# Optimization experiments

Hardware: AMD Instinct MI355X
Metric: run time of the kernel (lower is better)

## Reference

```python
import jax, jax.numpy as jnp
import numpy as np

C_IN = 128
C_INNER = 128


def setup_inputs() -> dict:
    key = jax.random.key(0)
    ks = jax.random.split(key, 9)
    b, c, h, w = 4, C_IN, 64, 64
    s = 1.0 / np.sqrt(c)
    x = jax.random.normal(ks[0], (b, c, h, w), dtype=jnp.float32)
    Wq = jax.random.normal(ks[1], (C_INNER, C_IN), dtype=jnp.float32) * s
    bq = jnp.zeros((C_INNER,), dtype=jnp.float32)
    Wk = jax.random.normal(ks[2], (C_INNER, C_IN), dtype=jnp.float32) * s
    bk = jnp.zeros((C_INNER,), dtype=jnp.float32)
    Wv = jax.random.normal(ks[3], (C_INNER, C_IN), dtype=jnp.float32) * s
    bv = jnp.zeros((C_INNER,), dtype=jnp.float32)
    Wo = jax.random.normal(ks[4], (C_IN, C_INNER), dtype=jnp.float32) * (1.0 / np.sqrt(C_INNER))
    bo = jnp.zeros((C_IN,), dtype=jnp.float32)
    return {"x": x, "Wq": Wq, "bq": bq, "Wk": Wk, "bk": bk,
            "Wv": Wv, "bv": bv, "Wo": Wo, "bo": bo}


def _conv1x1(x, W, bias):
    # x: (b,c,h,w), W: (o,c) -> (b,o,h,w)
    return jnp.einsum('oc,bchw->bohw', W, x) + bias[None, :, None, None]


def reference(x, Wq, bq, Wk, bk, Wv, bv, Wo, bo):
    b, c, h, w = x.shape
    ci = Wq.shape[0]
    n = h * w
    q = _conv1x1(x, Wq, bq).reshape(b, ci, n)          # (b, ci, n)
    k = _conv1x1(x, Wk, bk).reshape(b, ci, n)          # (b, ci, n)
    v = _conv1x1(x, Wv, bv).reshape(b, ci, n)          # (b, ci, n)
    # attn = softmax(q^T @ k) over keys
    attn = jnp.einsum('bci,bcj->bij', q, k)            # (b, n, n)
    attn = jax.nn.softmax(attn, axis=-1)
    out = jnp.einsum('bij,bcj->bci', attn, v)          # (b, ci, n)
    out = out.reshape(b, ci, h, w)
    out = _conv1x1(out, Wo, bo)
    return out + x
```

## Files before the change

### kernel.cpp

```cpp
#include <hip/hip_runtime.h>
#include <math.h>
#include <stdint.h>

#define CDIM 128
#define NTOT 4096

typedef _Float16 f16x8 __attribute__((ext_vector_type(8)));
typedef float floatx4 __attribute__((ext_vector_type(4)));

static __device__ __forceinline__ floatx4 mfma16(f16x8 a, f16x8 b, floatx4 c) {
    return __builtin_amdgcn_mfma_f32_16x16x32_f16(a, b, c, 0, 0, 0);
}
static __device__ __forceinline__ unsigned short f2h(float f) {
    _Float16 h = (_Float16)f;
    return __builtin_bit_cast(unsigned short, h);
}
static __device__ __forceinline__ float h2f(unsigned short u) {
    return (float)__builtin_bit_cast(_Float16, u);
}

#define SWZ(row, cc) ((((row) << 7)) + ((((cc) ^ ((row) & 15))) << 3))

__global__ __launch_bounds__(256) void qkv_proj_kernel(
    const float* __restrict__ x,
    const float* __restrict__ Wq, const float* __restrict__ bq,
    const float* __restrict__ Wk, const float* __restrict__ bk,
    const float* __restrict__ Wv, const float* __restrict__ bv,
    unsigned short* __restrict__ qo, unsigned short* __restrict__ ko,
    unsigned short* __restrict__ vo)
{
    __shared__ __align__(16) unsigned short Xs[64][136];
    __shared__ __align__(16) unsigned short Ws[64][136];

    const int t = threadIdx.x, b = blockIdx.y, n0 = blockIdx.x * 64;
    const int zo = blockIdx.z * 64;
    const int w = t >> 6, quad = (t >> 4) & 3, l15 = t & 15;

    {
        const int n = (t & 15) * 4;
        const int c = (t >> 4) * 8;
        float4 xr[8];
        #pragma unroll
        for (int j = 0; j < 8; ++j)
            xr[j] = *(const float4*)&x[((size_t)b * CDIM + c + j) * NTOT + n0 + n];
        #pragma unroll
        for (int k = 0; k < 4; ++k) {
            ushort4 ulo, uhi;
            ulo.x = f2h(((const float*)&xr[0])[k]);
            ulo.y = f2h(((const float*)&xr[1])[k]);
            ulo.z = f2h(((const float*)&xr[2])[k]);
            ulo.w = f2h(((const float*)&xr[3])[k]);
            uhi.x = f2h(((const float*)&xr[4])[k]);
            uhi.y = f2h(((const float*)&xr[5])[k]);
            uhi.z = f2h(((const float*)&xr[6])[k]);
            uhi.w = f2h(((const float*)&xr[7])[k]);
            *(ushort4*)&Xs[n + k][c]     = ulo;
            *(ushort4*)&Xs[n + k][c + 4] = uhi;
        }
    }

    f16x8 xf[4];
    for (int s = 0; s < 3; ++s) {
        const float* W    = (s == 0) ? Wq : (s == 1) ? Wk : Wv;
        const float* bias = (s == 0) ? bq : (s == 1) ? bk : bv;
        if (s) __syncthreads();
        {
            int o = t >> 2, ch = (t & 3) * 32;
            #pragma unroll
            for (int i = 0; i < 8; ++i) {
                float4 f4 = *(const float4*)&W[(size_t)(zo + o) * CDIM + ch + i * 4];
                ushort4 u = { f2h(f4.x), f2h(f4.y), f2h(f4.z), f2h(f4.w) };
                *(ushort4*)&Ws[o][ch + i * 4] = u;
            }
        }
        __syncthreads();
        if (s == 0) {
            #pragma unroll
            for (int f = 0; f < 4; ++f)
                xf[f] = *(const f16x8*)&Xs[w * 16 + l15][f * 32 + quad * 8];
        }

        if (s < 2) {
            unsigned short* dst = (s == 0) ? qo : ko;
            #pragma unroll
            for (int ot = 0; ot < 4; ++ot) {
                floatx4 acc = (floatx4){0.f, 0.f, 0.f, 0.f};
                #pragma unroll
                for (int f = 0; f < 4; ++f) {
                    f16x8 aW = *(const f16x8*)&Ws[ot * 16 + l15][f * 32 + quad * 8];
                    acc = mfma16(aW, xf[f], acc);
                }
                const int ob = zo + ot * 16 + quad * 4;
                ushort4 u;
                u.x = f2h(acc[0] + bias[ob + 0]);
                u.y = f2h(acc[1] + bias[ob + 1]);
                u.z = f2h(acc[2] + bias[ob + 2]);
                u.w = f2h(acc[3] + bias[ob + 3]);
                *(ushort4*)&dst[((size_t)b * NTOT + n0 + w * 16 + l15) * CDIM + ob] = u;
            }
        } else {
            #pragma unroll
            for (int ot = 0; ot < 4; ++ot) {
                floatx4 acc = (floatx4){0.f, 0.f, 0.f, 0.f};
                #pragma unroll
                for (int f = 0; f < 4; ++f) {
                    f16x8 bW = *(const f16x8*)&Ws[ot * 16 + l15][f * 32 + quad * 8];
                    acc = mfma16(xf[f], bW, acc);
                }
                const int o = zo + ot * 16 + l15;
                const float bv_ = bias[o];
                ushort4 u;
                u.x = f2h(acc[0] + bv_); u.y = f2h(acc[1] + bv_);
                u.z = f2h(acc[2] + bv_); u.w = f2h(acc[3] + bv_);
                *(ushort4*)&vo[((size_t)b * CDIM + o) * NTOT + n0 + w * 16 + quad * 4] = u;
            }
        }
    }
}

__global__ __launch_bounds__(256, 2) void attn_kernel(
    const unsigned short* __restrict__ qg,
    const unsigned short* __restrict__ kg,
    const unsigned short* __restrict__ vg,
    unsigned short* __restrict__ Op,
    float* __restrict__ Ms, float* __restrict__ Ls)
{
    __shared__ __align__(16) unsigned short Ks[128 * 128];
    __shared__ __align__(16) unsigned short Vs[128 * 128];

    const int t = threadIdx.x;
    const int w = t >> 6, quad = (t >> 4) & 3, l15 = t & 15;
    const int b = blockIdx.y;
    const int z = blockIdx.z;
    const int i0 = blockIdx.x * 128;
    const int jbase = z * 1024;
    const size_t vbase = (size_t)b * CDIM * NTOT;

    f16x8 bQ[2][4];
    #pragma unroll
    for (int nt = 0; nt < 2; ++nt) {
        const size_t qrow = ((size_t)b * NTOT + i0 + w * 32 + nt * 16 + l15) * CDIM;
        #pragma unroll
        for (int f = 0; f < 4; ++f)
            bQ[nt][f] = *(const f16x8*)&qg[qrow + f * 32 + quad * 8];
    }

    floatx4 accO[2][8];
    #pragma unroll
    for (int nt = 0; nt < 2; ++nt)
        #pragma unroll
        for (int dt = 0; dt < 8; ++dt) accO[nt][dt] = (floatx4){0.f, 0.f, 0.f, 0.f};
    float m_run[2] = {-INFINITY, -INFINITY};
    float l_part[2] = {0.f, 0.f};

    for (int iter = 0; iter < 8; ++iter) {
        const int j0 = jbase + iter * 128;
        __syncthreads();

        {
            const size_t kb_ = ((size_t)b * NTOT + j0) * CDIM;
            #pragma unroll
            for (int r = 0; r < 8; ++r) {
                int flat = r * 256 + t;
                int row = flat >> 4, cc = flat & 15;
                *(uint4*)&Ks[SWZ(row, cc)] =
                    *(const uint4*)&kg[kb_ + (size_t)row * CDIM + cc * 8];
                *(uint4*)&Vs[SWZ(row, cc)] =
                    *(const uint4*)&vg[vbase + (size_t)row * NTOT + j0 + cc * 8];
            }
        }
        __syncthreads();

        floatx4 accT[2][8];
        #pragma unroll
        for (int nt = 0; nt < 2; ++nt)
            #pragma unroll
            for (int jt = 0; jt < 8; ++jt) accT[nt][jt] = (floatx4){0.f, 0.f, 0.f, 0.f};
        #pragma unroll
        for (int jt = 0; jt < 8; ++jt)
            #pragma unroll
            for (int f = 0; f < 4; ++f) {
                f16x8 aK = *(const f16x8*)&Ks[SWZ(jt * 16 + l15, f * 4 + quad)];
                accT[0][jt] = mfma16(aK, bQ[0][f], accT[0][jt]);
                accT[1][jt] = mfma16(aK, bQ[1][f], accT[1][jt]);
            }

        float m_new[2], alpha[2];
        ushort4 pu[2][8];
        #pragma unroll
        for (int nt = 0; nt < 2; ++nt) {
            float tm = accT[nt][0][0];
            #pragma unroll
            for (int jt = 0; jt < 8; ++jt)
                #pragma unroll
                for (int r = 0; r < 4; ++r) tm = fmaxf(tm, accT[nt][jt][r]);
            tm = fmaxf(tm, __shfl_xor(tm, 16));
            tm = fmaxf(tm, __shfl_xor(tm, 32));
            m_new[nt] = fmaxf(m_run[nt], tm);
            alpha[nt] = __expf(m_run[nt] - m_new[nt]);
            m_run[nt] = m_new[nt];
            float ps = 0.f;
            #pragma unroll
            for (int jt = 0; jt < 8; ++jt) {
                float p0 = __expf(accT[nt][jt][0] - m_new[nt]);
                float p1 = __expf(accT[nt][jt][1] - m_new[nt]);
                float p2 = __expf(accT[nt][jt][2] - m_new[nt]);
                float p3 = __expf(accT[nt][jt][3] - m_new[nt]);
                ps += (p0 + p1) + (p2 + p3);
                pu[nt][jt].x = f2h(p0); pu[nt][jt].y = f2h(p1);
                pu[nt][jt].z = f2h(p2); pu[nt][jt].w = f2h(p3);
            }
            l_part[nt] = l_part[nt] * alpha[nt] + ps;
            #pragma unroll
            for (int dt = 0; dt < 8; ++dt) {
                accO[nt][dt][0] *= alpha[nt]; accO[nt][dt][1] *= alpha[nt];
                accO[nt][dt][2] *= alpha[nt]; accO[nt][dt][3] *= alpha[nt];
            }
        }

        __syncthreads();

        #pragma unroll
        for (int nt = 0; nt < 2; ++nt) {
            const int prow = w * 32 + nt * 16 + l15;
            #pragma unroll
            for (int jt = 0; jt < 8; ++jt)
                *(ushort4*)&Ks[SWZ(prow, 2 * jt + (quad >> 1)) + (quad & 1) * 4] =
                    pu[nt][jt];
        }

        f16x8 bP[2][4];
        #pragma unroll
        for (int nt = 0; nt < 2; ++nt) {
            const int prow = w * 32 + nt * 16 + l15;
            #pragma unroll
            for (int kb = 0; kb < 4; ++kb)
                bP[nt][kb] = *(const f16x8*)&Ks[SWZ(prow, kb * 4 + quad)];
        }
        #pragma unroll
        for (int dt = 0; dt < 8; ++dt)
            #pragma unroll
            for (int kb = 0; kb < 4; ++kb) {
                f16x8 aV = *(const f16x8*)&Vs[SWZ(dt * 16 + l15, kb * 4 + quad)];
                accO[0][dt] = mfma16(aV, bP[0][kb], accO[0][dt]);
                accO[1][dt] = mfma16(aV, bP[1][kb], accO[1][dt]);
            }
    }

    #pragma unroll
    for (int nt = 0; nt < 2; ++nt) {
        float lf = l_part[nt];
        lf += __shfl_xor(lf, 16);
        lf += __shfl_xor(lf, 32);
        const float inv = 1.0f / lf;
        const size_t orow =
            (((size_t)z * 4 + b) * NTOT + i0 + w * 32 + nt * 16 + l15) * CDIM;
        #pragma unroll
        for (int dt = 0; dt < 8; ++dt) {
            ushort4 u;
            u.x = f2h(accO[nt][dt][0] * inv); u.y = f2h(accO[nt][dt][1] * inv);
            u.z = f2h(accO[nt][dt][2] * inv); u.w = f2h(accO[nt][dt][3] * inv);
            *(ushort4*)&Op[orow + dt * 16 + quad * 4] = u;
        }
        if (quad == 0) {
            const int idx = (z * 4 + b) * NTOT + i0 + w * 32 + nt * 16 + l15;
            Ms[idx] = m_run[nt];
            Ls[idx] = lf;
        }
    }
}

__global__ __launch_bounds__(256) void out_proj_kernel(
    const unsigned short* __restrict__ Op,
    const float* __restrict__ Ms, const float* __restrict__ Ls,
    const float* __restrict__ Wo, const float* __restrict__ bo,
    const float* __restrict__ x, float* __restrict__ out)
{
    __shared__ __align__(16) unsigned short As[64][136];
    __shared__ __align__(16) unsigned short Ws[64][136];

    const int t = threadIdx.x, b = blockIdx.y, n0 = blockIdx.x * 64;
    const int zo = blockIdx.z * 64;
    const int w = t >> 6, quad = (t >> 4) & 3, l15 = t & 15;

    const size_t PER = (size_t)NTOT * 4 * CDIM;

    #pragma unroll
    for (int r = 0; r < 4; ++r) {
        int flat = r * 256 + t;
        int row = flat >> 4, c16 = (flat & 15) * 8;
        const int bn = b * NTOT + n0 + row;
        float m0 = Ms[bn], m1 = Ms[bn + 16384], m2 = Ms[bn + 32768], m3 = Ms[bn + 49152];
        float M = fmaxf(fmaxf(m0, m1), fmaxf(m2, m3));
        float w0 = Ls[bn]         * __expf(m0 - M);
        float w1 = Ls[bn + 16384] * __expf(m1 - M);
        float w2 = Ls[bn + 32768] * __expf(m2 - M);
        float w3 = Ls[bn + 49152] * __expf(m3 - M);
        const float inv = 1.0f / (w0 + w1 + w2 + w3);
        w0 *= inv; w1 *= inv; w2 *= inv; w3 *= inv;

        const size_t base = (size_t)bn * CDIM + c16;
        uint4 a0 = *(const uint4*)&Op[base];
        uint4 a1 = *(const uint4*)&Op[PER + base];
        uint4 a2 = *(const uint4*)&Op[2 * PER + base];
        uint4 a3 = *(const uint4*)&Op[3 * PER + base];
        const unsigned short* p0 = (const unsigned short*)&a0;
        const unsigned short* p1 = (const unsigned short*)&a1;
        const unsigned short* p2 = (const unsigned short*)&a2;
        const unsigned short* p3 = (const unsigned short*)&a3;
        unsigned short mv[8];
        #pragma unroll
        for (int j = 0; j < 8; ++j)
            mv[j] = f2h(w0 * h2f(p0[j]) + w1 * h2f(p1[j]) +
                        w2 * h2f(p2[j]) + w3 * h2f(p3[j]));
        *(uint4*)&As[row][c16] = *(const uint4*)mv;
    }
    {
        int o = t >> 2, ch = (t & 3) * 32;
        #pragma unroll
        for (int i = 0; i < 8; ++i) {
            float4 f4 = *(const float4*)&Wo[(size_t)(zo + o) * CDIM + ch + i * 4];
            ushort4 u = { f2h(f4.x), f2h(f4.y), f2h(f4.z), f2h(f4.w) };
            *(ushort4*)&Ws[o][ch + i * 4] = u;
        }
    }
    __syncthreads();

    f16x8 bA[4];
    #pragma unroll
    for (int f = 0; f < 4; ++f)
        bA[f] = *(const f16x8*)&As[w * 16 + l15][f * 32 + quad * 8];

    #pragma unroll
    for (int ot = 0; ot < 4; ++ot) {
        floatx4 acc = (floatx4){0.f, 0.f, 0.f, 0.f};
        #pragma unroll
        for (int f = 0; f < 4; ++f) {
            f16x8 aW = *(const f16x8*)&Ws[ot * 16 + l15][f * 32 + quad * 8];
            acc = mfma16(aW, bA[f], acc);
        }
        const int ob = zo + ot * 16 + quad * 4;
        #pragma unroll
        for (int r = 0; r < 4; ++r) {
            size_t idx = ((size_t)b * CDIM + ob + r) * NTOT + n0 + w * 16 + l15;
            out[idx] = acc[r] + bo[ob + r] + x[idx];
        }
    }
}

extern "C" void kernel_launch(void* const* d_in, const int* in_sizes, int n_in,
                              void* d_out, int out_size, void* d_ws, size_t ws_size,
                              hipStream_t stream)
{
    const float* x  = (const float*)d_in[0];
    const float* Wq = (const float*)d_in[1];
    const float* bq = (const float*)d_in[2];
    const float* Wk = (const float*)d_in[3];
    const float* bk = (const float*)d_in[4];
    const float* Wv = (const float*)d_in[5];
    const float* bv = (const float*)d_in[6];
    const float* Wo = (const float*)d_in[7];
    const float* bo = (const float*)d_in[8];
    float* out = (float*)d_out;

    const size_t PER = (size_t)4 * CDIM * NTOT;
    unsigned short* q_ws  = (unsigned short*)d_ws;
    unsigned short* k_ws  = q_ws + PER;
    unsigned short* v_ws  = k_ws + PER;
    unsigned short* op_ws = v_ws + PER;
    float*          ms_ws = (float*)(op_ws + 4 * PER);
    float*          ls_ws = ms_ws + 4 * 16384;

    qkv_proj_kernel<<<dim3(64, 4, 2), dim3(256), 0, stream>>>(
        x, Wq, bq, Wk, bk, Wv, bv, q_ws, k_ws, v_ws);
    attn_kernel<<<dim3(32, 4, 4), dim3(256), 0, stream>>>(
        q_ws, k_ws, v_ws, op_ws, ms_ws, ls_ws);
    out_proj_kernel<<<dim3(64, 4, 2), dim3(256), 0, stream>>>(
        op_ws, ms_ws, ls_ws, Wo, bo, x, out);
}
```

Measured before the change: 165.3 us.

## Double-buffer K/V tiles with async global-to-LDS loads and remap attention grid

The attention kernel now stages 64-key K/V tiles into two LDS buffers using global_load_lds direct copies, prefetching the next tile while computing on the current one, instead of synchronous 128-key loads through registers. The tile size halves so the loop runs 16 iterations, with a new 8-wide swizzle for the 64-column V and P layouts. The grid is flattened to 1D with a block-index swizzle to improve L2 locality across batches and key splits. The aim is to hide global-load latency and cut register staging, at the cost of more barriers and smaller MFMA work per iteration.

New measurement: 144.3 us. 12.7% less time.

```diff
diff --git a/kernel.cpp b/kernel.cpp
--- a/kernel.cpp
+++ b/kernel.cpp
@@ -20,6 +20,13 @@
 }
 
 #define SWZ(row, cc) ((((row) << 7)) + ((((cc) ^ ((row) & 15))) << 3))
+#define SWZ8(row, cc) ((((row) << 6)) + ((((cc) ^ ((row) & 7))) << 3))
+
+static __device__ __forceinline__ void gload_lds16(const void* g, void* l) {
+    __builtin_amdgcn_global_load_lds(
+        (const __attribute__((address_space(1))) void*)g,
+        (__attribute__((address_space(3))) void*)l, 16, 0, 0);
+}
 
 __global__ __launch_bounds__(256) void qkv_proj_kernel(
     const float* __restrict__ x,
@@ -125,14 +132,18 @@
     unsigned short* __restrict__ Op,
     float* __restrict__ Ms, float* __restrict__ Ls)
 {
-    __shared__ __align__(16) unsigned short Ks[128 * 128];
-    __shared__ __align__(16) unsigned short Vs[128 * 128];
+    __shared__ __align__(16) unsigned short Kb[2][64 * 128];
+    __shared__ __align__(16) unsigned short Vb[2][128 * 64];
 
     const int t = threadIdx.x;
     const int w = t >> 6, quad = (t >> 4) & 3, l15 = t & 15;
-    const int b = blockIdx.y;
-    const int z = blockIdx.z;
-    const int i0 = blockIdx.x * 128;
+
+    const int bid = blockIdx.x;
+    const int swz = ((bid & 7) << 6) | (bid >> 3);
+    const int gidx = swz >> 5;
+    const int b = gidx & 3;
+    const int z = gidx >> 2;
+    const int i0 = (swz & 31) * 128;
     const int jbase = z * 1024;
     const size_t vbase = (size_t)b * CDIM * NTOT;
 
@@ -144,6 +155,22 @@
         for (int f = 0; f < 4; ++f)
             bQ[nt][f] = *(const f16x8*)&qg[qrow + f * 32 + quad * 8];
     }
+
+    auto stage = [&](unsigned short* Kd, unsigned short* Vd, int j0) {
+        const size_t kbase = ((size_t)b * NTOT + j0) * CDIM;
+        const size_t vrow0 = vbase + j0;
+        #pragma unroll
+        for (int r = 0; r < 4; ++r) {
+            const int flat = r * 256 + t;
+            const int ldsoff = (r * 256 + (t & ~63)) * 8;
+            const int krow = flat >> 4, kcc = flat & 15;
+            gload_lds16(&kg[kbase + (size_t)krow * CDIM + ((kcc ^ (krow & 15)) << 3)],
+                        &Kd[ldsoff]);
+            const int vrow = flat >> 3, vcc = flat & 7;
+            gload_lds16(&vg[vrow0 + (size_t)vrow * NTOT + ((vcc ^ (vrow & 7)) << 3)],
+                        &Vd[ldsoff]);
+        }
+    };
 
     floatx4 accO[2][8];
     #pragma unroll
@@ -153,45 +180,37 @@
     float m_run[2] = {-INFINITY, -INFINITY};
     float l_part[2] = {0.f, 0.f};
 
-    for (int iter = 0; iter < 8; ++iter) {
-        const int j0 = jbase + iter * 128;
-        __syncthreads();
-
-        {
-            const size_t kb_ = ((size_t)b * NTOT + j0) * CDIM;
-            #pragma unroll
-            for (int r = 0; r < 8; ++r) {
-                int flat = r * 256 + t;
-                int row = flat >> 4, cc = flat & 15;
-                *(uint4*)&Ks[SWZ(row, cc)] =
-                    *(const uint4*)&kg[kb_ + (size_t)row * CDIM + cc * 8];
-                *(uint4*)&Vs[SWZ(row, cc)] =
-                    *(const uint4*)&vg[vbase + (size_t)row * NTOT + j0 + cc * 8];
-            }
-        }
-        __syncthreads();
-
-        floatx4 accT[2][8];
+    stage(Kb[0], Vb[0], jbase);
+
+    for (int iter = 0; iter < 16; ++iter) {
+        const int cur = iter & 1;
+
+        asm volatile("s_waitcnt vmcnt(0) lgkmcnt(0)" ::: "memory");
+        __builtin_amdgcn_s_barrier();
+
+        if (iter < 15) stage(Kb[cur ^ 1], Vb[cur ^ 1], jbase + (iter + 1) * 64);
+
+        floatx4 accT[2][4];
         #pragma unroll
         for (int nt = 0; nt < 2; ++nt)
             #pragma unroll
-            for (int jt = 0; jt < 8; ++jt) accT[nt][jt] = (floatx4){0.f, 0.f, 0.f, 0.f};
-        #pragma unroll
-        for (int jt = 0; jt < 8; ++jt)
+            for (int jt = 0; jt < 4; ++jt) accT[nt][jt] = (floatx4){0.f, 0.f, 0.f, 0.f};
+        #pragma unroll
+        for (int jt = 0; jt < 4; ++jt)
             #pragma unroll
             for (int f = 0; f < 4; ++f) {
-                f16x8 aK = *(const f16x8*)&Ks[SWZ(jt * 16 + l15, f * 4 + quad)];
+                f16x8 aK = *(const f16x8*)&Kb[cur][SWZ(jt * 16 + l15, f * 4 + quad)];
                 accT[0][jt] = mfma16(aK, bQ[0][f], accT[0][jt]);
                 accT[1][jt] = mfma16(aK, bQ[1][f], accT[1][jt]);
             }
 
         float m_new[2], alpha[2];
-        ushort4 pu[2][8];
+        ushort4 pu[2][4];
         #pragma unroll
         for (int nt = 0; nt < 2; ++nt) {
             float tm = accT[nt][0][0];
             #pragma unroll
-            for (int jt = 0; jt < 8; ++jt)
+            for (int jt = 0; jt < 4; ++jt)
                 #pragma unroll
                 for (int r = 0; r < 4; ++r) tm = fmaxf(tm, accT[nt][jt][r]);
             tm = fmaxf(tm, __shfl_xor(tm, 16));
@@ -201,7 +220,7 @@
             m_run[nt] = m_new[nt];
             float ps = 0.f;
             #pragma unroll
-            for (int jt = 0; jt < 8; ++jt) {
+            for (int jt = 0; jt < 4; ++jt) {
                 float p0 = __expf(accT[nt][jt][0] - m_new[nt]);
                 float p1 = __expf(accT[nt][jt][1] - m_new[nt]);
                 float p2 = __expf(accT[nt][jt][2] - m_new[nt]);
@@ -218,30 +237,32 @@
             }
         }
 
-        __syncthreads();
-
+        asm volatile("s_waitcnt lgkmcnt(0)" ::: "memory");
+        __builtin_amdgcn_s_barrier();
+
+        unsigned short* Pb = Kb[cur];
         #pragma unroll
         for (int nt = 0; nt < 2; ++nt) {
             const int prow = w * 32 + nt * 16 + l15;
             #pragma unroll
-            for (int jt = 0; jt < 8; ++jt)
-                *(ushort4*)&Ks[SWZ(prow, 2 * jt + (quad >> 1)) + (quad & 1) * 4] =
+            for (int jt = 0; jt < 4; ++jt)
+                *(ushort4*)&Pb[SWZ8(prow, 2 * jt + (quad >> 1)) + (quad & 1) * 4] =
                     pu[nt][jt];
         }
 
-        f16x8 bP[2][4];
+        f16x8 bP[2][2];
         #pragma unroll
         for (int nt = 0; nt < 2; ++nt) {
             const int prow = w * 32 + nt * 16 + l15;
             #pragma unroll
-            for (int kb = 0; kb < 4; ++kb)
-                bP[nt][kb] = *(const f16x8*)&Ks[SWZ(prow, kb * 4 + quad)];
+            for (int kb = 0; kb < 2; ++kb)
+                bP[nt][kb] = *(const f16x8*)&Pb[SWZ8(prow, kb * 4 + quad)];
         }
         #pragma unroll
         for (int dt = 0; dt < 8; ++dt)
             #pragma unroll
-            for (int kb = 0; kb < 4; ++kb) {
-                f16x8 aV = *(const f16x8*)&Vs[SWZ(dt * 16 + l15, kb * 4 + quad)];
+            for (int kb = 0; kb < 2; ++kb) {
+                f16x8 aV = *(const f16x8*)&Vb[cur][SWZ8(dt * 16 + l15, kb * 4 + quad)];
                 accO[0][dt] = mfma16(aV, bP[0][kb], accO[0][dt]);
                 accO[1][dt] = mfma16(aV, bP[1][kb], accO[1][dt]);
             }
@@ -373,7 +394,7 @@
 
     qkv_proj_kernel<<<dim3(64, 4, 2), dim3(256), 0, stream>>>(
         x, Wq, bq, Wk, bk, Wv, bv, q_ws, k_ws, v_ws);
-    attn_kernel<<<dim3(32, 4, 4), dim3(256), 0, stream>>>(
+    attn_kernel<<<dim3(512, 1, 1), dim3(256), 0, stream>>>(
         q_ws, k_ws, v_ws, op_ws, ms_ws, ls_ws);
     out_proj_kernel<<<dim3(64, 4, 2), dim3(256), 0, stream>>>(
         op_ws, ms_ws, ls_ws, Wo, bo, x, out);
```
